# Kernel tuning notes

Measured on AMD Instinct MI355X. Metric: run time of the kernel, lower is better.

The kernel has to match this reference:

```python
import jax, jax.numpy as jnp
import numpy as np

DIM, HEADS, KV_HEADS = 1024, 16, 4
B, T = 1, 4096
HEAD_DIM = DIM // HEADS           # 64
KV_DIM = DIM // (HEADS // KV_HEADS)  # 256
SCALE = HEAD_DIM ** -0.5


def setup_inputs() -> dict:
    key = jax.random.key(0)
    ks = jax.random.split(key, 9)
    s = lambda fan_in: fan_in ** -0.5
    return {
        "x": jax.random.normal(ks[0], (B, T, DIM), jnp.float32),
        "mask": jnp.tril(jnp.ones((1, 1, T, T), jnp.bool_)),  # causal
        "q_w": jax.random.normal(ks[1], (DIM, DIM), jnp.float32) * s(DIM),
        "q_b": jnp.zeros((DIM,), jnp.float32),
        "k_w": jax.random.normal(ks[2], (KV_DIM, DIM), jnp.float32) * s(DIM),
        "k_b": jnp.zeros((KV_DIM,), jnp.float32),
        "v_w": jax.random.normal(ks[3], (KV_DIM, DIM), jnp.float32) * s(DIM),
        "v_b": jnp.zeros((KV_DIM,), jnp.float32),
        "o_w": jax.random.normal(ks[4], (DIM, DIM), jnp.float32) * s(DIM),
        "o_b": jnp.zeros((DIM,), jnp.float32),
    }


def reference(x, mask, q_w, q_b, k_w, k_b, v_w, v_b, o_w, o_b):
    b, t, d = x.shape
    g = HEADS // KV_HEADS  # query heads per kv head
    # projections (torch Linear: x @ W^T + b)
    q = (x @ q_w.T + q_b).reshape(b, t, HEADS, HEAD_DIM).transpose(0, 2, 1, 3)      # [B,H,T,hd]
    k = (x @ k_w.T + k_b).reshape(b, t, KV_HEADS, HEAD_DIM).transpose(0, 2, 1, 3)   # [B,Hk,T,hd]
    v = (x @ v_w.T + v_b).reshape(b, t, KV_HEADS, HEAD_DIM).transpose(0, 2, 1, 3)   # [B,Hk,T,hd]
    # GQA: group query heads over shared kv heads
    qg = q.reshape(b, KV_HEADS, g, t, HEAD_DIM)                                     # [B,Hk,g,T,hd]
    scores = jnp.einsum('bkgtd,bksd->bkgts', qg, k) * SCALE                         # [B,Hk,g,T,T]
    scores = jnp.where(mask[:, :, None, :, :], scores, -1e9)
    attn = jax.nn.softmax(scores, axis=-1)  # dropout is identity in eval mode
    out = jnp.einsum('bkgts,bksd->bkgtd', attn, v)                                  # [B,Hk,g,T,hd]
    out = out.reshape(b, HEADS, t, HEAD_DIM).transpose(0, 2, 1, 3).reshape(b, t, d)
    out = out @ o_w.T + o_b
    return out, k, v  # (output, new kv cache)
```

## Files before the change

### kernel.cpp

```cpp
#include <hip/hip_runtime.h>
#include <hip/hip_bf16.h>
#include <stdint.h>

typedef __bf16 bf16;
typedef __bf16 bf16x8 __attribute__((ext_vector_type(8)));
typedef float  f32x4 __attribute__((ext_vector_type(4)));

#define SEQ   4096
#define DIM_  1024
#define HD_   64
#define NEG_BIG (-30000.0f)

__device__ __forceinline__ bf16x8 cvt8(const float* p) {
    f32x4 a = *(const f32x4*)p, b = *(const f32x4*)(p + 4);
    bf16x8 r;
    r[0]=(bf16)a[0]; r[1]=(bf16)a[1]; r[2]=(bf16)a[2]; r[3]=(bf16)a[3];
    r[4]=(bf16)b[0]; r[5]=(bf16)b[1]; r[6]=(bf16)b[2]; r[7]=(bf16)b[3];
    return r;
}

__device__ __forceinline__ void gload16(const bf16* g, bf16* l) {
    __builtin_amdgcn_global_load_lds(
        (const __attribute__((address_space(1))) void*)g,
        (__attribute__((address_space(3))) void*)l, 16, 0, 0);
}

__global__ __launch_bounds__(256)
void conv_bf16(const float* __restrict__ x,  const float* __restrict__ qw,
               const float* __restrict__ kw, const float* __restrict__ vw,
               const float* __restrict__ ow,
               bf16* __restrict__ xb,  bf16* __restrict__ qwb,
               bf16* __restrict__ kwb, bf16* __restrict__ vwb,
               bf16* __restrict__ owb)
{
    int b = blockIdx.x;
    const float* s; bf16* d; int base;
    if (b < 2048)      { s = x;  d = xb;  base = b * 2048; }
    else if (b < 2560) { s = qw; d = qwb; base = (b - 2048) * 2048; }
    else if (b < 2688) { s = kw; d = kwb; base = (b - 2560) * 2048; }
    else if (b < 2816) { s = vw; d = vwb; base = (b - 2688) * 2048; }
    else               { s = ow; d = owb; base = (b - 2816) * 2048; }
    int i = base + threadIdx.x * 8;
    *(bf16x8*)(d + i) = cvt8(s + i);
}

template<int MODE, bool BWBF>
__global__ __launch_bounds__(256)
void gemm_bt(const bf16* __restrict__ A,
             const void* __restrict__ B0, const float* __restrict__ b0,
             const void* __restrict__ B1, const float* __restrict__ b1,
             const void* __restrict__ B2, const float* __restrict__ b2,
             float* __restrict__ C0, float* __restrict__ C1, float* __restrict__ C2,
             bf16* __restrict__ Qbf, bf16* __restrict__ Kbf, bf16* __restrict__ VTbf)
{
    const int K = 1024;
    const int tid  = threadIdx.x;
    const int lane = tid & 63, wave = tid >> 6;
    const int qd = lane >> 4, ln = lane & 15;
    const int wm = (wave & 1) * 32, wn = (wave >> 1) * 64;
    const int m0 = blockIdx.x * 64, n0 = blockIdx.y * 128;

    const void* Bp; const float* bias;
    if (MODE == 1) {
        if (n0 < 1024)      { Bp = (const bf16*)B0 + (size_t)n0 * K;        bias = b0 + n0; }
        else if (n0 < 1280) { Bp = (const bf16*)B1 + (size_t)(n0-1024) * K; bias = b1 + (n0-1024); }
        else                { Bp = (const bf16*)B2 + (size_t)(n0-1280) * K; bias = b2 + (n0-1280); }
    } else if (BWBF)        { Bp = (const bf16*)B0 + (size_t)n0 * K;        bias = b0 + n0; }
    else                    { Bp = (const float*)B0 + (size_t)n0 * K;       bias = b0 + n0; }

    __shared__ bf16 As[64*32];
    __shared__ bf16 Bs[128*32];

    const int gr = lane >> 2, gc = (lane & 3) * 8;
    const bf16* Ag  = A + (size_t)(m0 + wave*16 + gr) * K + gc;
    bf16* AsW = As + wave*16*32;
    const bf16* Bg0 = (const bf16*)Bp + (size_t)(wave*32 + gr) * K + gc;
    const bf16* Bg1 = (const bf16*)Bp + (size_t)(wave*32 + 16 + gr) * K + gc;
    bf16* BsW0 = Bs + (wave*32) * 32;
    bf16* BsW1 = Bs + (wave*32 + 16) * 32;

    f32x4 acc[2][4] = {};

    for (int k0 = 0; k0 < K; k0 += 32) {
        if constexpr (MODE == 1 || BWBF) {
            __syncthreads();
            gload16(Ag  + k0, AsW);
            gload16(Bg0 + k0, BsW0);
            gload16(Bg1 + k0, BsW1);
            __syncthreads();
        } else {
            bf16x8 rb[2];
            #pragma unroll
            for (int i = 0; i < 2; ++i) {
                int s = i*256 + tid;
                int row = s >> 2, ch = s & 3;
                rb[i] = cvt8((const float*)Bp + (size_t)row*K + k0 + ch*8);
            }
            __syncthreads();
            gload16(Ag + k0, AsW);
            #pragma unroll
            for (int i = 0; i < 2; ++i) {
                int s = i*256 + tid;
                int row = s >> 2, ch = s & 3;
                *(bf16x8*)(Bs + row*32 + ch*8) = rb[i];
            }
            __syncthreads();
        }

        bf16x8 af[2], bg[4];
        #pragma unroll
        for (int i = 0; i < 2; ++i)
            af[i] = *(const bf16x8*)(As + (wm + i*16 + ln)*32 + qd*8);
        #pragma unroll
        for (int j = 0; j < 4; ++j)
            bg[j] = *(const bf16x8*)(Bs + (wn + j*16 + ln)*32 + qd*8);

        #pragma unroll
        for (int i = 0; i < 2; ++i)
            #pragma unroll
            for (int j = 0; j < 4; ++j)
                acc[i][j] = __builtin_amdgcn_mfma_f32_16x16x32_bf16(af[i], bg[j], acc[i][j], 0, 0, 0);
    }

    #pragma unroll
    for (int i = 0; i < 2; ++i) {
        #pragma unroll
        for (int j = 0; j < 4; ++j) {
            int colg = n0 + wn + j*16 + ln;
            float bv = bias[wn + j*16 + ln];
            #pragma unroll
            for (int r = 0; r < 4; ++r) {
                int rowg = m0 + wm + i*16 + qd*4 + r;
                float v = acc[i][j][r] + bv;
                if (MODE == 0) {
                    C0[(size_t)rowg*1024 + colg] = v;
                } else if (colg < 1024) {
                    Qbf[(size_t)rowg*1024 + colg] = (bf16)(v * 0.125f);
                } else if (colg < 1280) {
                    int c2 = colg - 1024;
                    size_t idx = (size_t)(c2 >> 6)*(SEQ*HD_) + (size_t)rowg*HD_ + (c2 & 63);
                    C1[idx]  = v;
                    Kbf[idx] = (bf16)v;
                } else {
                    int c2 = colg - 1280;
                    C2[(size_t)(c2 >> 6)*(SEQ*HD_) + (size_t)rowg*HD_ + (c2 & 63)] = v;
                    VTbf[(size_t)(c2 >> 6)*(HD_*SEQ) + (size_t)(c2 & 63)*SEQ + rowg] = (bf16)v;
                }
            }
        }
    }
}

__global__ __launch_bounds__(256)
void attn_fwd(const bf16* __restrict__ Q, const bf16* __restrict__ Kc,
              const bf16* __restrict__ VT, bf16* __restrict__ att)
{
    const int bid  = blockIdx.x;
    const int head = bid & 15;
    const int mt   = 63 - (bid >> 4);
    const int qb   = mt * 64;
    const int kvh  = head >> 2;

    const int tid = threadIdx.x, lane = tid & 63, wave = tid >> 6;
    const int qd = lane >> 4, ln = lane & 15;
    const int rw0 = qb + wave * 16;

    __shared__ bf16 Ks[64*72];
    __shared__ bf16 Vt[64*72];
    __shared__ bf16 Ps[4][16*72];

    const bf16* Kbase = Kc + (size_t)kvh * SEQ * HD_;
    const bf16* Vbase = VT + (size_t)kvh * HD_ * SEQ;

    bf16x8 aq[2];
    #pragma unroll
    for (int ks = 0; ks < 2; ++ks)
        aq[ks] = *(const bf16x8*)(Q + (size_t)(rw0 + ln)*DIM_ + head*HD_ + ks*32 + qd*8);

    f32x4 o[4] = {};
    float l_p[4] = {0.f, 0.f, 0.f, 0.f};

    const float LOG2E = 1.4426950408889634f;
    const float C16   = 16.0f * LOG2E;
    const int nkt = mt + 1;

    for (int kt = 0; kt < nkt; ++kt) {
        const int kb = kt * 64;

        bf16x8 rk[2], rv[2];
        #pragma unroll
        for (int i = 0; i < 2; ++i) {
            int s = i*256 + tid;
            int r8 = s >> 3, ch = s & 7;
            rk[i] = *(const bf16x8*)(Kbase + (size_t)(kb + r8)*HD_ + ch*8);
            rv[i] = *(const bf16x8*)(Vbase + (size_t)r8*SEQ + kb + ch*8);
        }
        __syncthreads();
        #pragma unroll
        for (int i = 0; i < 2; ++i) {
            int s = i*256 + tid;
            int r8 = s >> 3, ch = s & 7;
            *(bf16x8*)(Ks + r8*72 + ch*8) = rk[i];
            *(bf16x8*)(Vt + r8*72 + ch*8) = rv[i];
        }
        __syncthreads();

        f32x4 S[4] = {};
        #pragma unroll
        for (int ks = 0; ks < 2; ++ks) {
            bf16x8 bk[4];
            #pragma unroll
            for (int nf = 0; nf < 4; ++nf)
                bk[nf] = *(const bf16x8*)(Ks + (nf*16 + ln)*72 + ks*32 + qd*8);
            #pragma unroll
            for (int nf = 0; nf < 4; ++nf)
                S[nf] = __builtin_amdgcn_mfma_f32_16x16x32_bf16(aq[ks], bk[nf], S[nf], 0, 0, 0);
        }

        if (kt == nkt - 1) {
            #pragma unroll
            for (int nf = 0; nf < 4; ++nf) {
                int col = kb + nf*16 + ln;
                #pragma unroll
                for (int r = 0; r < 4; ++r) {
                    int row = rw0 + qd*4 + r;
                    if (col > row) S[nf][r] = NEG_BIG;
                }
            }
        }

        bf16* Pw = &Ps[wave][0];
        #pragma unroll
        for (int r = 0; r < 4; ++r) {
            #pragma unroll
            for (int nf = 0; nf < 4; ++nf) {
                float p = exp2f(S[nf][r] * LOG2E - C16);
                l_p[r] += p;
                Pw[(qd*4 + r)*72 + nf*16 + ln] = (bf16)p;
            }
        }
        asm volatile("s_waitcnt lgkmcnt(0)" ::: "memory");

        #pragma unroll
        for (int ks = 0; ks < 2; ++ks) {
            bf16x8 bv[4];
            #pragma unroll
            for (int nf = 0; nf < 4; ++nf)
                bv[nf] = *(const bf16x8*)(Vt + (nf*16 + ln)*72 + ks*32 + qd*8);
            bf16x8 ap = *(const bf16x8*)(&Ps[wave][ln*72 + ks*32 + qd*8]);
            #pragma unroll
            for (int nf = 0; nf < 4; ++nf)
                o[nf] = __builtin_amdgcn_mfma_f32_16x16x32_bf16(ap, bv[nf], o[nf], 0, 0, 0);
        }
    }

    #pragma unroll
    for (int r = 0; r < 4; ++r) {
        float l = l_p[r];
        l += __shfl_xor(l, 1);
        l += __shfl_xor(l, 2);
        l += __shfl_xor(l, 4);
        l += __shfl_xor(l, 8);
        float inv = 1.0f / l;
        int trow = rw0 + qd*4 + r;
        #pragma unroll
        for (int nf = 0; nf < 4; ++nf)
            att[(size_t)trow*DIM_ + head*HD_ + nf*16 + ln] = (bf16)(o[nf][r] * inv);
    }
}

extern "C" void kernel_launch(void* const* d_in, const int* in_sizes, int n_in,
                              void* d_out, int out_size, void* d_ws, size_t ws_size,
                              hipStream_t stream)
{
    const float* x  = (const float*)d_in[0];
    const float* qw = (const float*)d_in[2];
    const float* qb = (const float*)d_in[3];
    const float* kw = (const float*)d_in[4];
    const float* kb = (const float*)d_in[5];
    const float* vw = (const float*)d_in[6];
    const float* vb = (const float*)d_in[7];
    const float* ow = (const float*)d_in[8];
    const float* ob = (const float*)d_in[9];

    float* out  = (float*)d_out;
    float* kout = out  + (size_t)SEQ * DIM_;
    float* vout = kout + (size_t)4 * SEQ * HD_;

    bf16* q_bf  = (bf16*)d_out;
    bf16* k_bf  = q_bf  + (size_t)SEQ * DIM_;
    bf16* vT_bf = k_bf  + (size_t)4 * SEQ * HD_;
    bf16* qw_bf = vT_bf + (size_t)4 * HD_ * SEQ;
    bf16* kw_bf = qw_bf + (size_t)1024 * 1024;
    bf16* vw_bf = kw_bf + (size_t)256 * 1024;

    bf16* x_bf = (bf16*)d_ws;
    bf16* att  = (bf16*)d_ws;
    bool  owbf_ok = ws_size >= (size_t)(8*1024*1024 + 2*1024*1024);
    bf16* ow_bf = owbf_ok ? (bf16*)((char*)d_ws + (size_t)8*1024*1024) : nullptr;

    int convBlocks = 2816 + (owbf_ok ? 512 : 0);
    conv_bf16<<<convBlocks, 256, 0, stream>>>(x, qw, kw, vw, ow,
                                              x_bf, qw_bf, kw_bf, vw_bf, ow_bf);

    gemm_bt<1, true><<<dim3(64, 12), 256, 0, stream>>>(x_bf, qw_bf, qb, kw_bf, kb, vw_bf, vb,
                                                       nullptr, kout, vout,
                                                       q_bf, k_bf, vT_bf);
    attn_fwd<<<dim3(1024), 256, 0, stream>>>(q_bf, k_bf, vT_bf, att);
    if (owbf_ok)
        gemm_bt<0, true><<<dim3(64, 8), 256, 0, stream>>>(att, ow_bf, ob, nullptr, nullptr,
                                                          nullptr, nullptr, out, nullptr, nullptr,
                                                          nullptr, nullptr, nullptr);
    else
        gemm_bt<0, false><<<dim3(64, 8), 256, 0, stream>>>(att, ow, ob, nullptr, nullptr,
                                                           nullptr, nullptr, out, nullptr, nullptr,
                                                           nullptr, nullptr, nullptr);
}
```

Before: 254.6 us.

## Enlarge GEMM tiles to 128x128 and double-buffer LDS loads

Doubles the M tile of the projection GEMMs so each wave computes a 64x64 sub-tile, raising operand reuse per LDS load. For the bf16-weight path, adds two LDS buffers with the next K-slice prefetched while MFMAs run on the current one, which removes one barrier per iteration. The grid is halved, which lowers block-level parallelism on a large-CU device and raises register use from the larger accumulator array.

```diff
diff --git a/kernel.cpp b/kernel.cpp
--- a/kernel.cpp
+++ b/kernel.cpp
@@ -53,12 +53,12 @@
              float* __restrict__ C0, float* __restrict__ C1, float* __restrict__ C2,
              bf16* __restrict__ Qbf, bf16* __restrict__ Kbf, bf16* __restrict__ VTbf)
 {
-    const int K = 1024;
+    const int K = 1024, NT = 32;
     const int tid  = threadIdx.x;
     const int lane = tid & 63, wave = tid >> 6;
     const int qd = lane >> 4, ln = lane & 15;
-    const int wm = (wave & 1) * 32, wn = (wave >> 1) * 64;
-    const int m0 = blockIdx.x * 64, n0 = blockIdx.y * 128;
+    const int wm = (wave & 1) * 64, wn = (wave >> 1) * 64;
+    const int m0 = blockIdx.x * 128, n0 = blockIdx.y * 128;
 
     const void* Bp; const float* bias;
     if (MODE == 1) {
@@ -68,27 +68,50 @@
     } else if (BWBF)        { Bp = (const bf16*)B0 + (size_t)n0 * K;        bias = b0 + n0; }
     else                    { Bp = (const float*)B0 + (size_t)n0 * K;       bias = b0 + n0; }
 
-    __shared__ bf16 As[64*32];
-    __shared__ bf16 Bs[128*32];
+    __shared__ bf16 As[2][128*32];
+    __shared__ bf16 Bs[2][128*32];
 
     const int gr = lane >> 2, gc = (lane & 3) * 8;
-    const bf16* Ag  = A + (size_t)(m0 + wave*16 + gr) * K + gc;
-    bf16* AsW = As + wave*16*32;
-    const bf16* Bg0 = (const bf16*)Bp + (size_t)(wave*32 + gr) * K + gc;
-    const bf16* Bg1 = (const bf16*)Bp + (size_t)(wave*32 + 16 + gr) * K + gc;
-    bf16* BsW0 = Bs + (wave*32) * 32;
-    bf16* BsW1 = Bs + (wave*32 + 16) * 32;
-
-    f32x4 acc[2][4] = {};
-
-    for (int k0 = 0; k0 < K; k0 += 32) {
-        if constexpr (MODE == 1 || BWBF) {
+    const bf16* Ag = A + (size_t)(m0 + wave*32 + gr) * K + gc;
+    const int ldsW = (wave*32) * 32;
+
+    f32x4 acc[4][4] = {};
+
+    if constexpr (MODE == 1 || BWBF) {
+        const bf16* Bg = (const bf16*)Bp + (size_t)(wave*32 + gr) * K + gc;
+        gload16(Ag,                 &As[0][ldsW]);
+        gload16(Ag + (size_t)16*K,  &As[0][ldsW + 16*32]);
+        gload16(Bg,                 &Bs[0][ldsW]);
+        gload16(Bg + (size_t)16*K,  &Bs[0][ldsW + 16*32]);
+        __syncthreads();
+        int cur = 0;
+        for (int t = 0; t < NT; ++t) {
+            if (t + 1 < NT) {
+                const bf16* ag = Ag + (t+1)*32;
+                const bf16* bgp = Bg + (t+1)*32;
+                gload16(ag,                &As[cur^1][ldsW]);
+                gload16(ag + (size_t)16*K, &As[cur^1][ldsW + 16*32]);
+                gload16(bgp,               &Bs[cur^1][ldsW]);
+                gload16(bgp + (size_t)16*K,&Bs[cur^1][ldsW + 16*32]);
+            }
+            bf16x8 af[4], bg[4];
+            #pragma unroll
+            for (int i = 0; i < 4; ++i)
+                af[i] = *(const bf16x8*)(&As[cur][(wm + i*16 + ln)*32 + qd*8]);
+            #pragma unroll
+            for (int j = 0; j < 4; ++j)
+                bg[j] = *(const bf16x8*)(&Bs[cur][(wn + j*16 + ln)*32 + qd*8]);
+            #pragma unroll
+            for (int i = 0; i < 4; ++i)
+                #pragma unroll
+                for (int j = 0; j < 4; ++j)
+                    acc[i][j] = __builtin_amdgcn_mfma_f32_16x16x32_bf16(af[i], bg[j], acc[i][j], 0, 0, 0);
             __syncthreads();
-            gload16(Ag  + k0, AsW);
-            gload16(Bg0 + k0, BsW0);
-            gload16(Bg1 + k0, BsW1);
-            __syncthreads();
-        } else {
+            cur ^= 1;
+        }
+    } else {
+        for (int t = 0; t < NT; ++t) {
+            int k0 = t * 32;
             bf16x8 rb[2];
             #pragma unroll
             for (int i = 0; i < 2; ++i) {
@@ -97,33 +120,32 @@
                 rb[i] = cvt8((const float*)Bp + (size_t)row*K + k0 + ch*8);
             }
             __syncthreads();
-            gload16(Ag + k0, AsW);
+            gload16(Ag + k0,                &As[0][ldsW]);
+            gload16(Ag + k0 + (size_t)16*K, &As[0][ldsW + 16*32]);
             #pragma unroll
             for (int i = 0; i < 2; ++i) {
                 int s = i*256 + tid;
                 int row = s >> 2, ch = s & 3;
-                *(bf16x8*)(Bs + row*32 + ch*8) = rb[i];
+                *(bf16x8*)(&Bs[0][row*32 + ch*8]) = rb[i];
             }
             __syncthreads();
-        }
-
-        bf16x8 af[2], bg[4];
-        #pragma unroll
-        for (int i = 0; i < 2; ++i)
-            af[i] = *(const bf16x8*)(As + (wm + i*16 + ln)*32 + qd*8);
-        #pragma unroll
-        for (int j = 0; j < 4; ++j)
-            bg[j] = *(const bf16x8*)(Bs + (wn + j*16 + ln)*32 + qd*8);
-
-        #pragma unroll
-        for (int i = 0; i < 2; ++i)
+            bf16x8 af[4], bg[4];
+            #pragma unroll
+            for (int i = 0; i < 4; ++i)
+                af[i] = *(const bf16x8*)(&As[0][(wm + i*16 + ln)*32 + qd*8]);
             #pragma unroll
             for (int j = 0; j < 4; ++j)
-                acc[i][j] = __builtin_amdgcn_mfma_f32_16x16x32_bf16(af[i], bg[j], acc[i][j], 0, 0, 0);
+                bg[j] = *(const bf16x8*)(&Bs[0][(wn + j*16 + ln)*32 + qd*8]);
+            #pragma unroll
+            for (int i = 0; i < 4; ++i)
+                #pragma unroll
+                for (int j = 0; j < 4; ++j)
+                    acc[i][j] = __builtin_amdgcn_mfma_f32_16x16x32_bf16(af[i], bg[j], acc[i][j], 0, 0, 0);
+        }
     }
 
     #pragma unroll
-    for (int i = 0; i < 2; ++i) {
+    for (int i = 0; i < 4; ++i) {
         #pragma unroll
         for (int j = 0; j < 4; ++j) {
             int colg = n0 + wn + j*16 + ln;
@@ -303,16 +325,16 @@
     conv_bf16<<<convBlocks, 256, 0, stream>>>(x, qw, kw, vw, ow,
                                               x_bf, qw_bf, kw_bf, vw_bf, ow_bf);
 
-    gemm_bt<1, true><<<dim3(64, 12), 256, 0, stream>>>(x_bf, qw_bf, qb, kw_bf, kb, vw_bf, vb,
+    gemm_bt<1, true><<<dim3(32, 12), 256, 0, stream>>>(x_bf, qw_bf, qb, kw_bf, kb, vw_bf, vb,
                                                        nullptr, kout, vout,
                                                        q_bf, k_bf, vT_bf);
     attn_fwd<<<dim3(1024), 256, 0, stream>>>(q_bf, k_bf, vT_bf, att);
     if (owbf_ok)
-        gemm_bt<0, true><<<dim3(64, 8), 256, 0, stream>>>(att, ow_bf, ob, nullptr, nullptr,
+        gemm_bt<0, true><<<dim3(32, 8), 256, 0, stream>>>(att, ow_bf, ob, nullptr, nullptr,
                                                           nullptr, nullptr, out, nullptr, nullptr,
                                                           nullptr, nullptr, nullptr);
     else
-        gemm_bt<0, false><<<dim3(64, 8), 256, 0, stream>>>(att, ow, ob, nullptr, nullptr,
+        gemm_bt<0, false><<<dim3(32, 8), 256, 0, stream>>>(att, ow, ob, nullptr, nullptr,
                                                            nullptr, nullptr, out, nullptr, nullptr,
                                                            nullptr, nullptr, nullptr);
 }
```

Result: slower. 268.2 us (+5.3%).

## Double-buffer GEMM LDS loads, enlarge attention tiles, prefetch K/V, fold log2e into Q

Applied to the files above, without the earlier changes.

The projection GEMM now double-buffers its A/B LDS tiles, so the async global-to-LDS copy for the next k-step overlaps the MFMA work on the current one, with one barrier per step instead of two. The attention kernel moves to 128-row query tiles with 8 waves, sharing each K/V tile load across twice as many rows. It prefetches the next K/V tile into registers during the current step, and each wave skips fully masked tiles. The log2(e) factor is folded into the Q scale at projection time, which removes a multiply per score. The trade-offs are half as many attention blocks, idle waves on causal-skip iterations, and a change in Q rounding.

```diff
diff --git a/kernel.cpp b/kernel.cpp
--- a/kernel.cpp
+++ b/kernel.cpp
@@ -10,6 +10,8 @@
 #define DIM_  1024
 #define HD_   64
 #define NEG_BIG (-30000.0f)
+
+#define QSCALE (0.125f * 1.4426950408889634f)
 
 __device__ __forceinline__ bf16x8 cvt8(const float* p) {
     f32x4 a = *(const f32x4*)p, b = *(const f32x4*)(p + 4);
@@ -53,7 +55,7 @@
              float* __restrict__ C0, float* __restrict__ C1, float* __restrict__ C2,
              bf16* __restrict__ Qbf, bf16* __restrict__ Kbf, bf16* __restrict__ VTbf)
 {
-    const int K = 1024;
+    const int K = 1024, NT = 32;
     const int tid  = threadIdx.x;
     const int lane = tid & 63, wave = tid >> 6;
     const int qd = lane >> 4, ln = lane & 15;
@@ -68,27 +70,47 @@
     } else if (BWBF)        { Bp = (const bf16*)B0 + (size_t)n0 * K;        bias = b0 + n0; }
     else                    { Bp = (const float*)B0 + (size_t)n0 * K;       bias = b0 + n0; }
 
-    __shared__ bf16 As[64*32];
-    __shared__ bf16 Bs[128*32];
+    __shared__ bf16 As[2][64*32];
+    __shared__ bf16 Bs[2][128*32];
 
     const int gr = lane >> 2, gc = (lane & 3) * 8;
-    const bf16* Ag  = A + (size_t)(m0 + wave*16 + gr) * K + gc;
-    bf16* AsW = As + wave*16*32;
-    const bf16* Bg0 = (const bf16*)Bp + (size_t)(wave*32 + gr) * K + gc;
-    const bf16* Bg1 = (const bf16*)Bp + (size_t)(wave*32 + 16 + gr) * K + gc;
-    bf16* BsW0 = Bs + (wave*32) * 32;
-    bf16* BsW1 = Bs + (wave*32 + 16) * 32;
+    const bf16* Ag = A + (size_t)(m0 + wave*16 + gr) * K + gc;
+    const int aW = (wave*16) * 32;
+    const int bW = (wave*32) * 32;
 
     f32x4 acc[2][4] = {};
 
-    for (int k0 = 0; k0 < K; k0 += 32) {
-        if constexpr (MODE == 1 || BWBF) {
+    if constexpr (MODE == 1 || BWBF) {
+        const bf16* Bg = (const bf16*)Bp + (size_t)(wave*32 + gr) * K + gc;
+        gload16(Ag,                &As[0][aW]);
+        gload16(Bg,                &Bs[0][bW]);
+        gload16(Bg + (size_t)16*K, &Bs[0][bW + 16*32]);
+        __syncthreads();
+        int cur = 0;
+        for (int t = 0; t < NT; ++t) {
+            if (t + 1 < NT) {
+                gload16(Ag + (t+1)*32,                &As[cur^1][aW]);
+                gload16(Bg + (t+1)*32,                &Bs[cur^1][bW]);
+                gload16(Bg + (t+1)*32 + (size_t)16*K, &Bs[cur^1][bW + 16*32]);
+            }
+            bf16x8 af[2], bg[4];
+            #pragma unroll
+            for (int i = 0; i < 2; ++i)
+                af[i] = *(const bf16x8*)(&As[cur][(wm + i*16 + ln)*32 + qd*8]);
+            #pragma unroll
+            for (int j = 0; j < 4; ++j)
+                bg[j] = *(const bf16x8*)(&Bs[cur][(wn + j*16 + ln)*32 + qd*8]);
+            #pragma unroll
+            for (int i = 0; i < 2; ++i)
+                #pragma unroll
+                for (int j = 0; j < 4; ++j)
+                    acc[i][j] = __builtin_amdgcn_mfma_f32_16x16x32_bf16(af[i], bg[j], acc[i][j], 0, 0, 0);
             __syncthreads();
-            gload16(Ag  + k0, AsW);
-            gload16(Bg0 + k0, BsW0);
-            gload16(Bg1 + k0, BsW1);
-            __syncthreads();
-        } else {
+            cur ^= 1;
+        }
+    } else {
+        for (int t = 0; t < NT; ++t) {
+            int k0 = t * 32;
             bf16x8 rb[2];
             #pragma unroll
             for (int i = 0; i < 2; ++i) {
@@ -97,29 +119,27 @@
                 rb[i] = cvt8((const float*)Bp + (size_t)row*K + k0 + ch*8);
             }
             __syncthreads();
-            gload16(Ag + k0, AsW);
+            gload16(Ag + k0, &As[0][aW]);
             #pragma unroll
             for (int i = 0; i < 2; ++i) {
                 int s = i*256 + tid;
                 int row = s >> 2, ch = s & 3;
-                *(bf16x8*)(Bs + row*32 + ch*8) = rb[i];
+                *(bf16x8*)(&Bs[0][row*32 + ch*8]) = rb[i];
             }
             __syncthreads();
-        }
-
-        bf16x8 af[2], bg[4];
-        #pragma unroll
-        for (int i = 0; i < 2; ++i)
-            af[i] = *(const bf16x8*)(As + (wm + i*16 + ln)*32 + qd*8);
-        #pragma unroll
-        for (int j = 0; j < 4; ++j)
-            bg[j] = *(const bf16x8*)(Bs + (wn + j*16 + ln)*32 + qd*8);
-
-        #pragma unroll
-        for (int i = 0; i < 2; ++i)
+            bf16x8 af[2], bg[4];
+            #pragma unroll
+            for (int i = 0; i < 2; ++i)
+                af[i] = *(const bf16x8*)(&As[0][(wm + i*16 + ln)*32 + qd*8]);
             #pragma unroll
             for (int j = 0; j < 4; ++j)
-                acc[i][j] = __builtin_amdgcn_mfma_f32_16x16x32_bf16(af[i], bg[j], acc[i][j], 0, 0, 0);
+                bg[j] = *(const bf16x8*)(&Bs[0][(wn + j*16 + ln)*32 + qd*8]);
+            #pragma unroll
+            for (int i = 0; i < 2; ++i)
+                #pragma unroll
+                for (int j = 0; j < 4; ++j)
+                    acc[i][j] = __builtin_amdgcn_mfma_f32_16x16x32_bf16(af[i], bg[j], acc[i][j], 0, 0, 0);
+        }
     }
 
     #pragma unroll
@@ -135,7 +155,7 @@
                 if (MODE == 0) {
                     C0[(size_t)rowg*1024 + colg] = v;
                 } else if (colg < 1024) {
-                    Qbf[(size_t)rowg*1024 + colg] = (bf16)(v * 0.125f);
+                    Qbf[(size_t)rowg*1024 + colg] = (bf16)(v * QSCALE);
                 } else if (colg < 1280) {
                     int c2 = colg - 1024;
                     size_t idx = (size_t)(c2 >> 6)*(SEQ*HD_) + (size_t)rowg*HD_ + (c2 & 63);
@@ -151,14 +171,14 @@
     }
 }
 
-__global__ __launch_bounds__(256)
+__global__ __launch_bounds__(512)
 void attn_fwd(const bf16* __restrict__ Q, const bf16* __restrict__ Kc,
               const bf16* __restrict__ VT, bf16* __restrict__ att)
 {
     const int bid  = blockIdx.x;
     const int head = bid & 15;
-    const int mt   = 63 - (bid >> 4);
-    const int qb   = mt * 64;
+    const int mt   = 31 - (bid >> 4);
+    const int qb   = mt * 128;
     const int kvh  = head >> 2;
 
     const int tid = threadIdx.x, lane = tid & 63, wave = tid >> 6;
@@ -167,7 +187,7 @@
 
     __shared__ bf16 Ks[64*72];
     __shared__ bf16 Vt[64*72];
-    __shared__ bf16 Ps[4][16*72];
+    __shared__ bf16 Ps[8][16*72];
 
     const bf16* Kbase = Kc + (size_t)kvh * SEQ * HD_;
     const bf16* Vbase = VT + (size_t)kvh * HD_ * SEQ;
@@ -180,30 +200,27 @@
     f32x4 o[4] = {};
     float l_p[4] = {0.f, 0.f, 0.f, 0.f};
 
-    const float LOG2E = 1.4426950408889634f;
-    const float C16   = 16.0f * LOG2E;
-    const int nkt = mt + 1;
+    const float C16 = 16.0f * 1.4426950408889634f;
+    const int nkt = 2 * mt + 2;
+
+    const int r8 = tid >> 3, ch = tid & 7;
+
+    bf16x8 rk = *(const bf16x8*)(Kbase + (size_t)r8*HD_ + ch*8);
+    bf16x8 rv = *(const bf16x8*)(Vbase + (size_t)r8*SEQ + ch*8);
 
     for (int kt = 0; kt < nkt; ++kt) {
         const int kb = kt * 64;
 
-        bf16x8 rk[2], rv[2];
-        #pragma unroll
-        for (int i = 0; i < 2; ++i) {
-            int s = i*256 + tid;
-            int r8 = s >> 3, ch = s & 7;
-            rk[i] = *(const bf16x8*)(Kbase + (size_t)(kb + r8)*HD_ + ch*8);
-            rv[i] = *(const bf16x8*)(Vbase + (size_t)r8*SEQ + kb + ch*8);
-        }
         __syncthreads();
-        #pragma unroll
-        for (int i = 0; i < 2; ++i) {
-            int s = i*256 + tid;
-            int r8 = s >> 3, ch = s & 7;
-            *(bf16x8*)(Ks + r8*72 + ch*8) = rk[i];
-            *(bf16x8*)(Vt + r8*72 + ch*8) = rv[i];
+        *(bf16x8*)(Ks + r8*72 + ch*8) = rk;
+        *(bf16x8*)(Vt + r8*72 + ch*8) = rv;
+        if (kt + 1 < nkt) {
+            rk = *(const bf16x8*)(Kbase + (size_t)(kb + 64 + r8)*HD_ + ch*8);
+            rv = *(const bf16x8*)(Vbase + (size_t)r8*SEQ + kb + 64 + ch*8);
         }
         __syncthreads();
+
+        if (kb >= rw0 + 16) continue;
 
         f32x4 S[4] = {};
         #pragma unroll
@@ -217,7 +234,7 @@
                 S[nf] = __builtin_amdgcn_mfma_f32_16x16x32_bf16(aq[ks], bk[nf], S[nf], 0, 0, 0);
         }
 
-        if (kt == nkt - 1) {
+        if (kb + 63 > rw0) {
             #pragma unroll
             for (int nf = 0; nf < 4; ++nf) {
                 int col = kb + nf*16 + ln;
@@ -234,7 +251,7 @@
         for (int r = 0; r < 4; ++r) {
             #pragma unroll
             for (int nf = 0; nf < 4; ++nf) {
-                float p = exp2f(S[nf][r] * LOG2E - C16);
+                float p = exp2f(S[nf][r] - C16);
                 l_p[r] += p;
                 Pw[(qd*4 + r)*72 + nf*16 + ln] = (bf16)p;
             }
@@ -306,7 +323,7 @@
     gemm_bt<1, true><<<dim3(64, 12), 256, 0, stream>>>(x_bf, qw_bf, qb, kw_bf, kb, vw_bf, vb,
                                                        nullptr, kout, vout,
                                                        q_bf, k_bf, vT_bf);
-    attn_fwd<<<dim3(1024), 256, 0, stream>>>(q_bf, k_bf, vT_bf, att);
+    attn_fwd<<<dim3(512), 512, 0, stream>>>(q_bf, k_bf, vT_bf, att);
     if (owbf_ok)
         gemm_bt<0, true><<<dim3(64, 8), 256, 0, stream>>>(att, ow_bf, ob, nullptr, nullptr,
                                                           nullptr, nullptr, out, nullptr, nullptr,
```

Result: slower. 266.4 us (+4.6%).

## Load GEMM fragments directly from global with register double-buffering; fold log2e into Q

Applied to the files above, without the earlier changes.

The projection GEMMs drop shared-memory staging and barriers. Each wave now loads its MFMA operand fragments straight from global memory into registers, double-buffered across k-steps so loads overlap the matrix multiplies. Separately, log2(e) is folded into the Q scaling so the softmax skips one multiply per score. The trade-off is that operand tiles are no longer shared across waves, which raises global/L2 traffic and register use, and the fp32 B path converts in registers on every load.

```diff
diff --git a/kernel.cpp b/kernel.cpp
--- a/kernel.cpp
+++ b/kernel.cpp
@@ -10,6 +10,8 @@
 #define DIM_  1024
 #define HD_   64
 #define NEG_BIG (-30000.0f)
+
+#define QSCALE (0.125f * 1.4426950408889634f)
 
 __device__ __forceinline__ bf16x8 cvt8(const float* p) {
     f32x4 a = *(const f32x4*)p, b = *(const f32x4*)(p + 4);
@@ -17,12 +19,6 @@
     r[0]=(bf16)a[0]; r[1]=(bf16)a[1]; r[2]=(bf16)a[2]; r[3]=(bf16)a[3];
     r[4]=(bf16)b[0]; r[5]=(bf16)b[1]; r[6]=(bf16)b[2]; r[7]=(bf16)b[3];
     return r;
-}
-
-__device__ __forceinline__ void gload16(const bf16* g, bf16* l) {
-    __builtin_amdgcn_global_load_lds(
-        (const __attribute__((address_space(1))) void*)g,
-        (__attribute__((address_space(3))) void*)l, 16, 0, 0);
 }
 
 __global__ __launch_bounds__(256)
@@ -60,66 +56,54 @@
     const int wm = (wave & 1) * 32, wn = (wave >> 1) * 64;
     const int m0 = blockIdx.x * 64, n0 = blockIdx.y * 128;
 
-    const void* Bp; const float* bias;
+    const float* bias;
+    const bf16*  Bb  = nullptr;
+    const float* Bbf = nullptr;
     if (MODE == 1) {
-        if (n0 < 1024)      { Bp = (const bf16*)B0 + (size_t)n0 * K;        bias = b0 + n0; }
-        else if (n0 < 1280) { Bp = (const bf16*)B1 + (size_t)(n0-1024) * K; bias = b1 + (n0-1024); }
-        else                { Bp = (const bf16*)B2 + (size_t)(n0-1280) * K; bias = b2 + (n0-1280); }
-    } else if (BWBF)        { Bp = (const bf16*)B0 + (size_t)n0 * K;        bias = b0 + n0; }
-    else                    { Bp = (const float*)B0 + (size_t)n0 * K;       bias = b0 + n0; }
-
-    __shared__ bf16 As[64*32];
-    __shared__ bf16 Bs[128*32];
-
-    const int gr = lane >> 2, gc = (lane & 3) * 8;
-    const bf16* Ag  = A + (size_t)(m0 + wave*16 + gr) * K + gc;
-    bf16* AsW = As + wave*16*32;
-    const bf16* Bg0 = (const bf16*)Bp + (size_t)(wave*32 + gr) * K + gc;
-    const bf16* Bg1 = (const bf16*)Bp + (size_t)(wave*32 + 16 + gr) * K + gc;
-    bf16* BsW0 = Bs + (wave*32) * 32;
-    bf16* BsW1 = Bs + (wave*32 + 16) * 32;
+        const bf16* W;
+        if (n0 < 1024)      { W = (const bf16*)B0 + (size_t)n0 * K;        bias = b0 + n0; }
+        else if (n0 < 1280) { W = (const bf16*)B1 + (size_t)(n0-1024) * K; bias = b1 + (n0-1024); }
+        else                { W = (const bf16*)B2 + (size_t)(n0-1280) * K; bias = b2 + (n0-1280); }
+        Bb = W + (size_t)(wn + ln) * K + qd*8;
+    } else if (BWBF) {
+        Bb  = (const bf16*)B0 + (size_t)(n0 + wn + ln) * K + qd*8;  bias = b0 + n0;
+    } else {
+        Bbf = (const float*)B0 + (size_t)(n0 + wn + ln) * K + qd*8; bias = b0 + n0;
+    }
+    const bf16* Ab = A + (size_t)(m0 + wm + ln) * K + qd*8;
 
     f32x4 acc[2][4] = {};
-
-    for (int k0 = 0; k0 < K; k0 += 32) {
+    bf16x8 aA[2], bA[4], aB[2], bB[4];
+
+    auto loadfr = [&](bf16x8 (&af)[2], bf16x8 (&bf_)[4], int k0) {
+        #pragma unroll
+        for (int i = 0; i < 2; ++i)
+            af[i] = *(const bf16x8*)(Ab + (size_t)i*16*K + k0);
         if constexpr (MODE == 1 || BWBF) {
-            __syncthreads();
-            gload16(Ag  + k0, AsW);
-            gload16(Bg0 + k0, BsW0);
-            gload16(Bg1 + k0, BsW1);
-            __syncthreads();
+            #pragma unroll
+            for (int j = 0; j < 4; ++j)
+                bf_[j] = *(const bf16x8*)(Bb + (size_t)j*16*K + k0);
         } else {
-            bf16x8 rb[2];
-            #pragma unroll
-            for (int i = 0; i < 2; ++i) {
-                int s = i*256 + tid;
-                int row = s >> 2, ch = s & 3;
-                rb[i] = cvt8((const float*)Bp + (size_t)row*K + k0 + ch*8);
-            }
-            __syncthreads();
-            gload16(Ag + k0, AsW);
-            #pragma unroll
-            for (int i = 0; i < 2; ++i) {
-                int s = i*256 + tid;
-                int row = s >> 2, ch = s & 3;
-                *(bf16x8*)(Bs + row*32 + ch*8) = rb[i];
-            }
-            __syncthreads();
-        }
-
-        bf16x8 af[2], bg[4];
+            #pragma unroll
+            for (int j = 0; j < 4; ++j)
+                bf_[j] = cvt8(Bbf + (size_t)j*16*K + k0);
+        }
+    };
+    auto domfma = [&](bf16x8 (&af)[2], bf16x8 (&bf_)[4]) {
         #pragma unroll
         for (int i = 0; i < 2; ++i)
-            af[i] = *(const bf16x8*)(As + (wm + i*16 + ln)*32 + qd*8);
-        #pragma unroll
-        for (int j = 0; j < 4; ++j)
-            bg[j] = *(const bf16x8*)(Bs + (wn + j*16 + ln)*32 + qd*8);
-
-        #pragma unroll
-        for (int i = 0; i < 2; ++i)
             #pragma unroll
             for (int j = 0; j < 4; ++j)
-                acc[i][j] = __builtin_amdgcn_mfma_f32_16x16x32_bf16(af[i], bg[j], acc[i][j], 0, 0, 0);
+                acc[i][j] = __builtin_amdgcn_mfma_f32_16x16x32_bf16(af[i], bf_[j], acc[i][j], 0, 0, 0);
+    };
+
+    loadfr(aA, bA, 0);
+    #pragma unroll 1
+    for (int t = 0; t < 32; t += 2) {
+        loadfr(aB, bB, (t + 1) * 32);
+        domfma(aA, bA);
+        if (t + 2 < 32) loadfr(aA, bA, (t + 2) * 32);
+        domfma(aB, bB);
     }
 
     #pragma unroll
@@ -135,7 +119,7 @@
                 if (MODE == 0) {
                     C0[(size_t)rowg*1024 + colg] = v;
                 } else if (colg < 1024) {
-                    Qbf[(size_t)rowg*1024 + colg] = (bf16)(v * 0.125f);
+                    Qbf[(size_t)rowg*1024 + colg] = (bf16)(v * QSCALE);
                 } else if (colg < 1280) {
                     int c2 = colg - 1024;
                     size_t idx = (size_t)(c2 >> 6)*(SEQ*HD_) + (size_t)rowg*HD_ + (c2 & 63);
@@ -180,8 +164,7 @@
     f32x4 o[4] = {};
     float l_p[4] = {0.f, 0.f, 0.f, 0.f};
 
-    const float LOG2E = 1.4426950408889634f;
-    const float C16   = 16.0f * LOG2E;
+    const float C16 = 16.0f * 1.4426950408889634f;
     const int nkt = mt + 1;
 
     for (int kt = 0; kt < nkt; ++kt) {
@@ -234,7 +217,7 @@
         for (int r = 0; r < 4; ++r) {
             #pragma unroll
             for (int nf = 0; nf < 4; ++nf) {
-                float p = exp2f(S[nf][r] * LOG2E - C16);
+                float p = exp2f(S[nf][r] - C16);
                 l_p[r] += p;
                 Pw[(qd*4 + r)*72 + nf*16 + ln] = (bf16)p;
             }
```

New measurement: 323.4 us. 27.0% more time.
